# Optimization experiments

Hardware: AMD Instinct MI355X
Metric: run time of the kernel (lower is better)

The kernel has to match this reference:

```python
import jax, jax.numpy as jnp
import numpy as np

B, C, H, W = 16, 512, 14, 14
OUT = 8192
EPS_SQRT = 1e-5
EPS_NORM = 1e-12


def _make_sketch(key, input_dim, output_dim):
    kh, ks = jax.random.split(key)
    rand_h = jax.random.randint(kh, (input_dim,), 0, output_dim)
    rand_s = (2 * jax.random.randint(ks, (input_dim,), 0, 2) - 1).astype(jnp.float32)
    # count-sketch matrix densified: one nonzero (+-1) per row
    S = jnp.zeros((input_dim, output_dim), dtype=jnp.float32)
    return S.at[jnp.arange(input_dim), rand_h].set(rand_s)


def setup_inputs() -> dict:
    key = jax.random.key(0)
    kx, k1, k2 = jax.random.split(key, 3)
    x = jax.random.normal(kx, (B, C, H, W), dtype=jnp.float32)
    sketch1 = _make_sketch(k1, C, OUT)
    sketch2 = _make_sketch(k2, C, OUT)
    return {"x": x, "sketch1": sketch1, "sketch2": sketch2}


def reference(x, sketch1, sketch2):
    output_dim = sketch1.shape[1]
    # [B,C,H,W] -> [B,H,W,C] then project with count-sketch matrices -> [B,H,W,OUT]
    xp = jnp.transpose(x, (0, 2, 3, 1))
    p1 = xp @ sketch1
    p2 = xp @ sketch2
    # circular convolution via FFT (torch.rfft unnormalized; torch.irfft has 1/n, then *output_dim)
    f1 = jnp.fft.rfft(p1, axis=-1)
    f2 = jnp.fft.rfft(p2, axis=-1)
    cbp = jnp.fft.irfft(f1 * f2, n=output_dim, axis=-1) * output_dim
    # sum-pool over spatial dims -> [B, OUT]
    X = cbp.sum(axis=(1, 2))
    # signed square-root
    X = jnp.sign(X) * jnp.sqrt(jnp.abs(X) + EPS_SQRT)
    # L2 normalize per row (F.normalize semantics)
    norm = jnp.maximum(jnp.linalg.norm(X, axis=-1, keepdims=True), EPS_NORM)
    return X / norm
```

## Files before the change

kernel.cpp:

```cpp
#include <hip/hip_runtime.h>
#include <math.h>

#define OUT_DIM 8192
#define C_DIM   512
#define B_DIM   16
#define HW      196

typedef __attribute__((ext_vector_type(8))) short bf16x8;
typedef __attribute__((ext_vector_type(4))) float f32x4;


__global__ __launch_bounds__(256) void prep(
    const float* __restrict__ x,
    const float* __restrict__ S1, const float* __restrict__ S2,
    int* __restrict__ h1, float* __restrict__ s1,
    int* __restrict__ h2, float* __restrict__ s2,
    unsigned short* __restrict__ PH, unsigned short* __restrict__ PLo,
    float* __restrict__ ss)
{
    const int bid = blockIdx.x;
    const int t = threadIdx.x;

    if (bid < 1024) {
        int row = bid & 511;
        const float* S = (bid < 512) ? S1 : S2;
        int* h = (bid < 512) ? h1 : h2;
        float* s = (bid < 512) ? s1 : s2;
        const float4* p = (const float4*)(S + (size_t)row * OUT_DIM);
#pragma unroll
        for (int m = 0; m < 8; ++m) {
            int q = t + m * 256;
            float4 v = p[q];
            int base = q * 4;
            if (v.x != 0.f) { h[row] = base + 0; s[row] = v.x; }
            if (v.y != 0.f) { h[row] = base + 1; s[row] = v.y; }
            if (v.z != 0.f) { h[row] = base + 2; s[row] = v.z; }
            if (v.w != 0.f) { h[row] = base + 3; s[row] = v.w; }
        }
        if (bid == 0 && t < B_DIM) ss[t] = 0.f;
        return;
    }

    const int u = bid - 1024;
    const int b = u >> 5, rb = u & 31;
    __shared__ float xs[16 * HW];
    const float* src = x + ((size_t)b * C_DIM + rb * 16) * HW;
#pragma unroll
    for (int i = 0; i < 13; ++i) {
        int idx = t + i * 256;
        if (idx < 16 * HW) xs[idx] = src[idx];
    }
    __syncthreads();

    const int r = t & 15, u0 = t >> 4;
#pragma unroll
    for (int p = 0; p < 2; ++p) {
        int unit = u0 + p * 16;
        if (unit < 28) {
            bf16x8 hv, lv;
#pragma unroll
            for (int e = 0; e < 8; ++e) {
                int k = unit * 8 + e;
                float v = (k < HW) ? xs[r * HW + k] : 0.f;
                unsigned int uv = __float_as_uint(v);
                unsigned short hi = (unsigned short)(uv >> 16);
                float hif = __uint_as_float(((unsigned int)hi) << 16);
                hv[e] = (short)hi;
                lv[e] = (short)(__float_as_uint(v - hif) >> 16);
            }
            int kb = unit >> 2, lk = unit & 3;
            size_t base = ((((size_t)b * 32 + rb) * 7 + kb) * 4 + lk) * 128 + r * 8;
            *(bf16x8*)(PH + base) = hv;
            *(bf16x8*)(PLo + base) = lv;
        }
    }
}

__global__ __launch_bounds__(256) void gram_mfma(
    const unsigned short* __restrict__ PH, const unsigned short* __restrict__ PLo,
    const int* __restrict__ h1, const float* __restrict__ s1,
    const int* __restrict__ h2, const float* __restrict__ s2,
    float* __restrict__ partials)
{
    __shared__ float bins[OUT_DIM];

    const int bid = blockIdx.x;
    const int xcd = bid & 7;
    const int idx = bid >> 3;
    const int b   = xcd + 8 * (idx & 1);
    const int tile = idx >> 1;
    const int c1b = (tile >> 2) * 128, c2b = (tile & 3) * 128;

    const int t = threadIdx.x;
    const int l = t & 63, w = t >> 6;
    const int wr = w >> 1, wc = w & 1;

    for (int mm = t; mm < OUT_DIM; mm += 256) bins[mm] = 0.f;

    const size_t arb0 = ((size_t)b * 32 + (c1b >> 4) + wr * 4) * 7;
    const size_t brb0 = ((size_t)b * 32 + (c2b >> 4) + wc * 4) * 7;
    const int loff = l * 8;

#define FRAG(P, rbase, m, kb) (*(const bf16x8*)((P) + ((rbase) + (size_t)(m) * 7 + (kb)) * 512 + loff))

    f32x4 acc[4][4];
#pragma unroll
    for (int m = 0; m < 4; ++m)
#pragma unroll
        for (int n = 0; n < 4; ++n) acc[m][n] = (f32x4){0.f, 0.f, 0.f, 0.f};

    bf16x8 ah[2][4], al[2][4], bh[2][4], bl[2][4];
#pragma unroll
    for (int m = 0; m < 4; ++m) {
        ah[0][m] = FRAG(PH,  arb0, m, 0);
        al[0][m] = FRAG(PLo, arb0, m, 0);
        bh[0][m] = FRAG(PH,  brb0, m, 0);
        bl[0][m] = FRAG(PLo, brb0, m, 0);
    }

#pragma unroll
    for (int kb = 0; kb < 7; ++kb) {
        const int cur = kb & 1, nxt = cur ^ 1;
        if (kb < 6) {
#pragma unroll
            for (int m = 0; m < 4; ++m) {
                ah[nxt][m] = FRAG(PH,  arb0, m, kb + 1);
                al[nxt][m] = FRAG(PLo, arb0, m, kb + 1);
                bh[nxt][m] = FRAG(PH,  brb0, m, kb + 1);
                bl[nxt][m] = FRAG(PLo, brb0, m, kb + 1);
            }
        }
#pragma unroll
        for (int m = 0; m < 4; ++m)
#pragma unroll
            for (int n = 0; n < 4; ++n) {
                acc[m][n] = __builtin_amdgcn_mfma_f32_16x16x32_bf16(ah[cur][m], bh[cur][n], acc[m][n], 0, 0, 0);
                acc[m][n] = __builtin_amdgcn_mfma_f32_16x16x32_bf16(ah[cur][m], bl[cur][n], acc[m][n], 0, 0, 0);
                acc[m][n] = __builtin_amdgcn_mfma_f32_16x16x32_bf16(al[cur][m], bh[cur][n], acc[m][n], 0, 0, 0);
            }
    }
#undef FRAG

    const int lrow = l & 15, lk = l >> 4;
    int   hh1[4][4]; float sv1[4][4];
    int   hh2[4];    float sv2[4];
#pragma unroll
    for (int m = 0; m < 4; ++m)
#pragma unroll
        for (int r = 0; r < 4; ++r) {
            int c1 = c1b + wr * 64 + m * 16 + lk * 4 + r;
            hh1[m][r] = h1[c1]; sv1[m][r] = s1[c1];
        }
#pragma unroll
    for (int n = 0; n < 4; ++n) {
        int c2 = c2b + wc * 64 + n * 16 + lrow;
        hh2[n] = h2[c2]; sv2[n] = s2[c2];
    }

    __syncthreads();
#pragma unroll
    for (int m = 0; m < 4; ++m)
#pragma unroll
        for (int n = 0; n < 4; ++n)
#pragma unroll
            for (int r = 0; r < 4; ++r) {
                int bin = (hh1[m][r] + hh2[n]) & (OUT_DIM - 1);
                atomicAdd(&bins[bin], acc[m][n][r] * sv1[m][r] * sv2[n]);
            }
    __syncthreads();

    float* outp = partials + (size_t)(b * 16 + tile) * OUT_DIM;
    for (int mm = t; mm < OUT_DIM; mm += 256) outp[mm] = bins[mm];
}

__global__ __launch_bounds__(256) void fin_a(
    float* __restrict__ partials, float* __restrict__ ss)
{
    const int b = blockIdx.x >> 4, ch = blockIdx.x & 15, t = threadIdx.x;
    float sq = 0.f;
    float vals[2];
    int ks[2];
#pragma unroll
    for (int i = 0; i < 2; ++i) {
        int k = ch * 512 + i * 256 + t;
        ks[i] = k;
        float a = 0.f;
#pragma unroll
        for (int tile = 0; tile < 16; ++tile)
            a += partials[(size_t)(b * 16 + tile) * OUT_DIM + k];
        a *= (float)OUT_DIM;
        float sg = (a > 0.f) ? 1.f : ((a < 0.f) ? -1.f : 0.f);
        vals[i] = sg * sqrtf(fabsf(a) + 1e-5f);
        sq += fabsf(a) + 1e-5f;
    }
#pragma unroll
    for (int off = 32; off; off >>= 1) sq += __shfl_down(sq, off, 64);
    __shared__ float red[4];
    if ((t & 63) == 0) red[t >> 6] = sq;
    __syncthreads();
    if (t == 0) atomicAdd(&ss[b], red[0] + red[1] + red[2] + red[3]);
#pragma unroll
    for (int i = 0; i < 2; ++i)
        partials[(size_t)(b * 16) * OUT_DIM + ks[i]] = vals[i];
}

__global__ __launch_bounds__(256) void fin_b(
    const float* __restrict__ partials, const float* __restrict__ ss,
    float* __restrict__ out)
{
    const int b = blockIdx.x >> 4, ch = blockIdx.x & 15, t = threadIdx.x;
    float inv = 1.f / fmaxf(sqrtf(ss[b]), 1e-12f);
#pragma unroll
    for (int i = 0; i < 2; ++i) {
        int k = ch * 512 + i * 256 + t;
        out[(size_t)b * OUT_DIM + k] = partials[(size_t)(b * 16) * OUT_DIM + k] * inv;
    }
}

extern "C" void kernel_launch(void* const* d_in, const int* in_sizes, int n_in,
                              void* d_out, int out_size, void* d_ws, size_t ws_size,
                              hipStream_t stream) {
    const float* x   = (const float*)d_in[0];
    const float* sk1 = (const float*)d_in[1];
    const float* sk2 = (const float*)d_in[2];

    char* ws = (char*)d_ws;
    int*   h1 = (int*)(ws);
    float* s1 = (float*)(ws + 2048);
    int*   h2 = (int*)(ws + 4096);
    float* s2 = (float*)(ws + 6144);
    float* ss = (float*)(ws + 8192);
    float* partials = (float*)(ws + 8448);
    unsigned short* PH  = (unsigned short*)(ws + 8397056);
    unsigned short* PLo = (unsigned short*)(ws + 15737088);

    prep<<<1536, 256, 0, stream>>>(x, sk1, sk2, h1, s1, h2, s2, PH, PLo, ss);
    gram_mfma<<<256, 256, 0, stream>>>(PH, PLo, h1, s1, h2, s2, partials);
    fin_a<<<256, 256, 0, stream>>>(partials, ss);
    fin_b<<<256, 256, 0, stream>>>(partials, ss, (float*)d_out);
}
```

Measured before the change: 121.1 us.

## Fuse finalization into gram kernel via last-block counter and widen to 512 threads

Folds the two finalization kernels into the gram kernel. A per-batch atomic counter picks the last of the 16 tile blocks, which sums the partials, applies the signed square root and the L2 normalization, and writes the output, removing two kernel launches. The gram kernel now runs 8 waves per block with half the N-tile each, giving more parallelism per block and fewer registers per thread. The cost is that only 16 blocks do the serialized final reduction, and cross-block visibility depends on threadfence. The squared norm is now computed from the rounded root values rather than from abs plus epsilon.

```diff
diff --git a/kernel.cpp b/kernel.cpp
--- a/kernel.cpp
+++ b/kernel.cpp
@@ -16,7 +16,7 @@
     int* __restrict__ h1, float* __restrict__ s1,
     int* __restrict__ h2, float* __restrict__ s2,
     unsigned short* __restrict__ PH, unsigned short* __restrict__ PLo,
-    float* __restrict__ ss)
+    int* __restrict__ cnt)
 {
     const int bid = blockIdx.x;
     const int t = threadIdx.x;
@@ -37,7 +37,7 @@
             if (v.z != 0.f) { h[row] = base + 2; s[row] = v.z; }
             if (v.w != 0.f) { h[row] = base + 3; s[row] = v.w; }
         }
-        if (bid == 0 && t < B_DIM) ss[t] = 0.f;
+        if (bid == 0 && t < B_DIM) cnt[t] = 0;
         return;
     }
 
@@ -76,13 +76,16 @@
     }
 }
 
-__global__ __launch_bounds__(256) void gram_mfma(
+__global__ __launch_bounds__(512) void gram_fused(
     const unsigned short* __restrict__ PH, const unsigned short* __restrict__ PLo,
     const int* __restrict__ h1, const float* __restrict__ s1,
     const int* __restrict__ h2, const float* __restrict__ s2,
-    float* __restrict__ partials)
+    float* __restrict__ partials, int* __restrict__ cnt,
+    float* __restrict__ out)
 {
     __shared__ float bins[OUT_DIM];
+    __shared__ float red[8];
+    __shared__ int lastflag;
 
     const int bid = blockIdx.x;
     const int xcd = bid & 7;
@@ -93,29 +96,32 @@
 
     const int t = threadIdx.x;
     const int l = t & 63, w = t >> 6;
-    const int wr = w >> 1, wc = w & 1;
-
-    for (int mm = t; mm < OUT_DIM; mm += 256) bins[mm] = 0.f;
+    const int wr = w >> 2, wc = w & 3;
+
+    for (int mm = t; mm < OUT_DIM; mm += 512) bins[mm] = 0.f;
 
     const size_t arb0 = ((size_t)b * 32 + (c1b >> 4) + wr * 4) * 7;
-    const size_t brb0 = ((size_t)b * 32 + (c2b >> 4) + wc * 4) * 7;
+    const size_t brb0 = ((size_t)b * 32 + (c2b >> 4) + wc * 2) * 7;
     const int loff = l * 8;
 
 #define FRAG(P, rbase, m, kb) (*(const bf16x8*)((P) + ((rbase) + (size_t)(m) * 7 + (kb)) * 512 + loff))
 
-    f32x4 acc[4][4];
+    f32x4 acc[4][2];
 #pragma unroll
     for (int m = 0; m < 4; ++m)
 #pragma unroll
-        for (int n = 0; n < 4; ++n) acc[m][n] = (f32x4){0.f, 0.f, 0.f, 0.f};
-
-    bf16x8 ah[2][4], al[2][4], bh[2][4], bl[2][4];
+        for (int n = 0; n < 2; ++n) acc[m][n] = (f32x4){0.f, 0.f, 0.f, 0.f};
+
+    bf16x8 ah[2][4], al[2][4], bh[2][2], bl[2][2];
 #pragma unroll
     for (int m = 0; m < 4; ++m) {
         ah[0][m] = FRAG(PH,  arb0, m, 0);
         al[0][m] = FRAG(PLo, arb0, m, 0);
-        bh[0][m] = FRAG(PH,  brb0, m, 0);
-        bl[0][m] = FRAG(PLo, brb0, m, 0);
+    }
+#pragma unroll
+    for (int n = 0; n < 2; ++n) {
+        bh[0][n] = FRAG(PH,  brb0, n, 0);
+        bl[0][n] = FRAG(PLo, brb0, n, 0);
     }
 
 #pragma unroll
@@ -126,14 +132,17 @@
             for (int m = 0; m < 4; ++m) {
                 ah[nxt][m] = FRAG(PH,  arb0, m, kb + 1);
                 al[nxt][m] = FRAG(PLo, arb0, m, kb + 1);
-                bh[nxt][m] = FRAG(PH,  brb0, m, kb + 1);
-                bl[nxt][m] = FRAG(PLo, brb0, m, kb + 1);
+            }
+#pragma unroll
+            for (int n = 0; n < 2; ++n) {
+                bh[nxt][n] = FRAG(PH,  brb0, n, kb + 1);
+                bl[nxt][n] = FRAG(PLo, brb0, n, kb + 1);
             }
         }
 #pragma unroll
         for (int m = 0; m < 4; ++m)
 #pragma unroll
-            for (int n = 0; n < 4; ++n) {
+            for (int n = 0; n < 2; ++n) {
                 acc[m][n] = __builtin_amdgcn_mfma_f32_16x16x32_bf16(ah[cur][m], bh[cur][n], acc[m][n], 0, 0, 0);
                 acc[m][n] = __builtin_amdgcn_mfma_f32_16x16x32_bf16(ah[cur][m], bl[cur][n], acc[m][n], 0, 0, 0);
                 acc[m][n] = __builtin_amdgcn_mfma_f32_16x16x32_bf16(al[cur][m], bh[cur][n], acc[m][n], 0, 0, 0);
@@ -143,7 +152,7 @@
 
     const int lrow = l & 15, lk = l >> 4;
     int   hh1[4][4]; float sv1[4][4];
-    int   hh2[4];    float sv2[4];
+    int   hh2[2];    float sv2[2];
 #pragma unroll
     for (int m = 0; m < 4; ++m)
 #pragma unroll
@@ -152,8 +161,8 @@
             hh1[m][r] = h1[c1]; sv1[m][r] = s1[c1];
         }
 #pragma unroll
-    for (int n = 0; n < 4; ++n) {
-        int c2 = c2b + wc * 64 + n * 16 + lrow;
+    for (int n = 0; n < 2; ++n) {
+        int c2 = c2b + wc * 32 + n * 16 + lrow;
         hh2[n] = h2[c2]; sv2[n] = s2[c2];
     }
 
@@ -161,7 +170,7 @@
 #pragma unroll
     for (int m = 0; m < 4; ++m)
 #pragma unroll
-        for (int n = 0; n < 4; ++n)
+        for (int n = 0; n < 2; ++n)
 #pragma unroll
             for (int r = 0; r < 4; ++r) {
                 int bin = (hh1[m][r] + hh2[n]) & (OUT_DIM - 1);
@@ -170,50 +179,51 @@
     __syncthreads();
 
     float* outp = partials + (size_t)(b * 16 + tile) * OUT_DIM;
-    for (int mm = t; mm < OUT_DIM; mm += 256) outp[mm] = bins[mm];
-}
-
-__global__ __launch_bounds__(256) void fin_a(
-    float* __restrict__ partials, float* __restrict__ ss)
-{
-    const int b = blockIdx.x >> 4, ch = blockIdx.x & 15, t = threadIdx.x;
+    for (int mm = t; mm < OUT_DIM; mm += 512) outp[mm] = bins[mm];
+
+    __threadfence();
+    __syncthreads();
+    if (t == 0) lastflag = (atomicAdd(&cnt[b], 1) == 15);
+    __syncthreads();
+    if (!lastflag) return;
+    __threadfence();
+
+    const float4* p4 = (const float4*)(partials + (size_t)b * 16 * OUT_DIM);
+    float4 va[4];
     float sq = 0.f;
-    float vals[2];
-    int ks[2];
-#pragma unroll
-    for (int i = 0; i < 2; ++i) {
-        int k = ch * 512 + i * 256 + t;
-        ks[i] = k;
-        float a = 0.f;
-#pragma unroll
-        for (int tile = 0; tile < 16; ++tile)
-            a += partials[(size_t)(b * 16 + tile) * OUT_DIM + k];
-        a *= (float)OUT_DIM;
-        float sg = (a > 0.f) ? 1.f : ((a < 0.f) ? -1.f : 0.f);
-        vals[i] = sg * sqrtf(fabsf(a) + 1e-5f);
-        sq += fabsf(a) + 1e-5f;
+#pragma unroll
+    for (int i = 0; i < 4; ++i) {
+        int q = t + i * 512;
+        float4 s = make_float4(0.f, 0.f, 0.f, 0.f);
+#pragma unroll
+        for (int tl = 0; tl < 16; ++tl) {
+            float4 v = p4[tl * 2048 + q];
+            s.x += v.x; s.y += v.y; s.z += v.z; s.w += v.w;
+        }
+        float comp[4] = {s.x, s.y, s.z, s.w};
+#pragma unroll
+        for (int e = 0; e < 4; ++e) {
+            float a = comp[e] * (float)OUT_DIM;
+            float sg = (a > 0.f) ? 1.f : ((a < 0.f) ? -1.f : 0.f);
+            comp[e] = sg * sqrtf(fabsf(a) + 1e-5f);
+            sq += comp[e] * comp[e];
+        }
+        va[i] = make_float4(comp[0], comp[1], comp[2], comp[3]);
     }
 #pragma unroll
     for (int off = 32; off; off >>= 1) sq += __shfl_down(sq, off, 64);
-    __shared__ float red[4];
-    if ((t & 63) == 0) red[t >> 6] = sq;
-    __syncthreads();
-    if (t == 0) atomicAdd(&ss[b], red[0] + red[1] + red[2] + red[3]);
-#pragma unroll
-    for (int i = 0; i < 2; ++i)
-        partials[(size_t)(b * 16) * OUT_DIM + ks[i]] = vals[i];
-}
-
-__global__ __launch_bounds__(256) void fin_b(
-    const float* __restrict__ partials, const float* __restrict__ ss,
-    float* __restrict__ out)
-{
-    const int b = blockIdx.x >> 4, ch = blockIdx.x & 15, t = threadIdx.x;
-    float inv = 1.f / fmaxf(sqrtf(ss[b]), 1e-12f);
-#pragma unroll
-    for (int i = 0; i < 2; ++i) {
-        int k = ch * 512 + i * 256 + t;
-        out[(size_t)b * OUT_DIM + k] = partials[(size_t)(b * 16) * OUT_DIM + k] * inv;
+    if (l == 0) red[w] = sq;
+    __syncthreads();
+    float tot = 0.f;
+#pragma unroll
+    for (int i = 0; i < 8; ++i) tot += red[i];
+    float inv = 1.f / fmaxf(sqrtf(tot), 1e-12f);
+
+    float4* o4 = (float4*)(out + (size_t)b * OUT_DIM);
+#pragma unroll
+    for (int i = 0; i < 4; ++i) {
+        int q = t + i * 512;
+        o4[q] = make_float4(va[i].x * inv, va[i].y * inv, va[i].z * inv, va[i].w * inv);
     }
 }
 
@@ -229,13 +239,11 @@
     float* s1 = (float*)(ws + 2048);
     int*   h2 = (int*)(ws + 4096);
     float* s2 = (float*)(ws + 6144);
-    float* ss = (float*)(ws + 8192);
+    int*   cnt = (int*)(ws + 8192);
     float* partials = (float*)(ws + 8448);
     unsigned short* PH  = (unsigned short*)(ws + 8397056);
     unsigned short* PLo = (unsigned short*)(ws + 15737088);
 
-    prep<<<1536, 256, 0, stream>>>(x, sk1, sk2, h1, s1, h2, s2, PH, PLo, ss);
-    gram_mfma<<<256, 256, 0, stream>>>(PH, PLo, h1, s1, h2, s2, partials);
-    fin_a<<<256, 256, 0, stream>>>(partials, ss);
-    fin_b<<<256, 256, 0, stream>>>(partials, ss, (float*)d_out);
+    prep<<<1536, 256, 0, stream>>>(x, sk1, sk2, h1, s1, h2, s2, PH, PLo, cnt);
+    gram_fused<<<256, 512, 0, stream>>>(PH, PLo, h1, s1, h2, s2, partials, cnt, (float*)d_out);
 }
```

After: 158.1 us. 1.31x slower.

## Split gram K-loop across two wave halves and merge finalize kernels

Applied to the files above, without the earlier changes.

The gram kernel now runs 512 threads per block. Two groups of four waves each take half of the padded K range (8 blocks instead of 7, zero-padded), and both halves accumulate atomically into the same shared-memory bins. This doubles the waves available per CU to hide load latency. prep pads the bf16 layout to 8 k-blocks and drops the ss zeroing. The two finalize kernels are merged into one kernel with one 1024-thread block per batch, which removes a launch and the global atomic normalization pass. In exchange there are more shared-memory atomics, and the finalize runs on only 16 blocks.

```diff
diff --git a/kernel.cpp b/kernel.cpp
--- a/kernel.cpp
+++ b/kernel.cpp
@@ -15,8 +15,7 @@
     const float* __restrict__ S1, const float* __restrict__ S2,
     int* __restrict__ h1, float* __restrict__ s1,
     int* __restrict__ h2, float* __restrict__ s2,
-    unsigned short* __restrict__ PH, unsigned short* __restrict__ PLo,
-    float* __restrict__ ss)
+    unsigned short* __restrict__ PH, unsigned short* __restrict__ PLo)
 {
     const int bid = blockIdx.x;
     const int t = threadIdx.x;
@@ -37,7 +36,6 @@
             if (v.z != 0.f) { h[row] = base + 2; s[row] = v.z; }
             if (v.w != 0.f) { h[row] = base + 3; s[row] = v.w; }
         }
-        if (bid == 0 && t < B_DIM) ss[t] = 0.f;
         return;
     }
 
@@ -56,27 +54,25 @@
 #pragma unroll
     for (int p = 0; p < 2; ++p) {
         int unit = u0 + p * 16;
-        if (unit < 28) {
-            bf16x8 hv, lv;
-#pragma unroll
-            for (int e = 0; e < 8; ++e) {
-                int k = unit * 8 + e;
-                float v = (k < HW) ? xs[r * HW + k] : 0.f;
-                unsigned int uv = __float_as_uint(v);
-                unsigned short hi = (unsigned short)(uv >> 16);
-                float hif = __uint_as_float(((unsigned int)hi) << 16);
-                hv[e] = (short)hi;
-                lv[e] = (short)(__float_as_uint(v - hif) >> 16);
-            }
-            int kb = unit >> 2, lk = unit & 3;
-            size_t base = ((((size_t)b * 32 + rb) * 7 + kb) * 4 + lk) * 128 + r * 8;
-            *(bf16x8*)(PH + base) = hv;
-            *(bf16x8*)(PLo + base) = lv;
-        }
-    }
-}
-
-__global__ __launch_bounds__(256) void gram_mfma(
+        bf16x8 hv, lv;
+#pragma unroll
+        for (int e = 0; e < 8; ++e) {
+            int k = unit * 8 + e;
+            float v = (k < HW) ? xs[r * HW + k] : 0.f;
+            unsigned int uv = __float_as_uint(v);
+            unsigned short hi = (unsigned short)(uv >> 16);
+            float hif = __uint_as_float(((unsigned int)hi) << 16);
+            hv[e] = (short)hi;
+            lv[e] = (short)(__float_as_uint(v - hif) >> 16);
+        }
+        int kb = unit >> 2, lk = unit & 3;
+        size_t base = ((((size_t)b * 32 + rb) * 8 + kb) * 4 + lk) * 128 + r * 8;
+        *(bf16x8*)(PH + base) = hv;
+        *(bf16x8*)(PLo + base) = lv;
+    }
+}
+
+__global__ __launch_bounds__(512, 2) void gram_mfma(
     const unsigned short* __restrict__ PH, const unsigned short* __restrict__ PLo,
     const int* __restrict__ h1, const float* __restrict__ s1,
     const int* __restrict__ h2, const float* __restrict__ s2,
@@ -93,15 +89,17 @@
 
     const int t = threadIdx.x;
     const int l = t & 63, w = t >> 6;
-    const int wr = w >> 1, wc = w & 1;
-
-    for (int mm = t; mm < OUT_DIM; mm += 256) bins[mm] = 0.f;
-
-    const size_t arb0 = ((size_t)b * 32 + (c1b >> 4) + wr * 4) * 7;
-    const size_t brb0 = ((size_t)b * 32 + (c2b >> 4) + wc * 4) * 7;
+    const int half = w >> 2;
+    const int wr = (w >> 1) & 1, wc = w & 1;
+
+    for (int mm = t; mm < OUT_DIM; mm += 512) bins[mm] = 0.f;
+
+    const int arb = b * 32 + (c1b >> 4) + wr * 4;
+    const int brb = b * 32 + (c2b >> 4) + wc * 4;
     const int loff = l * 8;
-
-#define FRAG(P, rbase, m, kb) (*(const bf16x8*)((P) + ((rbase) + (size_t)(m) * 7 + (kb)) * 512 + loff))
+    const int kb0 = half * 4;
+
+#define FRAG(P, rb, kb) (*(const bf16x8*)((P) + ((size_t)((rb) * 8 + (kb)) * 512) + loff))
 
     f32x4 acc[4][4];
 #pragma unroll
@@ -112,22 +110,23 @@
     bf16x8 ah[2][4], al[2][4], bh[2][4], bl[2][4];
 #pragma unroll
     for (int m = 0; m < 4; ++m) {
-        ah[0][m] = FRAG(PH,  arb0, m, 0);
-        al[0][m] = FRAG(PLo, arb0, m, 0);
-        bh[0][m] = FRAG(PH,  brb0, m, 0);
-        bl[0][m] = FRAG(PLo, brb0, m, 0);
-    }
-
-#pragma unroll
-    for (int kb = 0; kb < 7; ++kb) {
-        const int cur = kb & 1, nxt = cur ^ 1;
-        if (kb < 6) {
+        ah[0][m] = FRAG(PH,  arb + m, kb0);
+        al[0][m] = FRAG(PLo, arb + m, kb0);
+        bh[0][m] = FRAG(PH,  brb + m, kb0);
+        bl[0][m] = FRAG(PLo, brb + m, kb0);
+    }
+
+#pragma unroll
+    for (int i = 0; i < 4; ++i) {
+        const int cur = i & 1, nxt = cur ^ 1;
+        if (i < 3) {
+            const int kn = kb0 + i + 1;
 #pragma unroll
             for (int m = 0; m < 4; ++m) {
-                ah[nxt][m] = FRAG(PH,  arb0, m, kb + 1);
-                al[nxt][m] = FRAG(PLo, arb0, m, kb + 1);
-                bh[nxt][m] = FRAG(PH,  brb0, m, kb + 1);
-                bl[nxt][m] = FRAG(PLo, brb0, m, kb + 1);
+                ah[nxt][m] = FRAG(PH,  arb + m, kn);
+                al[nxt][m] = FRAG(PLo, arb + m, kn);
+                bh[nxt][m] = FRAG(PH,  brb + m, kn);
+                bl[nxt][m] = FRAG(PLo, brb + m, kn);
             }
         }
 #pragma unroll
@@ -170,51 +169,40 @@
     __syncthreads();
 
     float* outp = partials + (size_t)(b * 16 + tile) * OUT_DIM;
-    for (int mm = t; mm < OUT_DIM; mm += 256) outp[mm] = bins[mm];
-}
-
-__global__ __launch_bounds__(256) void fin_a(
-    float* __restrict__ partials, float* __restrict__ ss)
+    for (int mm = t; mm < OUT_DIM; mm += 512) outp[mm] = bins[mm];
+}
+
+__global__ __launch_bounds__(1024) void fin(
+    const float* __restrict__ partials, float* __restrict__ out)
 {
-    const int b = blockIdx.x >> 4, ch = blockIdx.x & 15, t = threadIdx.x;
+    const int b = blockIdx.x, t = threadIdx.x;
+    const float* pb = partials + (size_t)b * 16 * OUT_DIM;
+    float v[8];
     float sq = 0.f;
-    float vals[2];
-    int ks[2];
-#pragma unroll
-    for (int i = 0; i < 2; ++i) {
-        int k = ch * 512 + i * 256 + t;
-        ks[i] = k;
+#pragma unroll
+    for (int i = 0; i < 8; ++i) {
+        int k = t + i * 1024;
         float a = 0.f;
 #pragma unroll
-        for (int tile = 0; tile < 16; ++tile)
-            a += partials[(size_t)(b * 16 + tile) * OUT_DIM + k];
+        for (int tl = 0; tl < 16; ++tl)
+            a += pb[tl * OUT_DIM + k];
         a *= (float)OUT_DIM;
         float sg = (a > 0.f) ? 1.f : ((a < 0.f) ? -1.f : 0.f);
-        vals[i] = sg * sqrtf(fabsf(a) + 1e-5f);
+        v[i] = sg * sqrtf(fabsf(a) + 1e-5f);
         sq += fabsf(a) + 1e-5f;
     }
 #pragma unroll
     for (int off = 32; off; off >>= 1) sq += __shfl_down(sq, off, 64);
-    __shared__ float red[4];
+    __shared__ float red[16];
     if ((t & 63) == 0) red[t >> 6] = sq;
     __syncthreads();
-    if (t == 0) atomicAdd(&ss[b], red[0] + red[1] + red[2] + red[3]);
-#pragma unroll
-    for (int i = 0; i < 2; ++i)
-        partials[(size_t)(b * 16) * OUT_DIM + ks[i]] = vals[i];
-}
-
-__global__ __launch_bounds__(256) void fin_b(
-    const float* __restrict__ partials, const float* __restrict__ ss,
-    float* __restrict__ out)
-{
-    const int b = blockIdx.x >> 4, ch = blockIdx.x & 15, t = threadIdx.x;
-    float inv = 1.f / fmaxf(sqrtf(ss[b]), 1e-12f);
-#pragma unroll
-    for (int i = 0; i < 2; ++i) {
-        int k = ch * 512 + i * 256 + t;
-        out[(size_t)b * OUT_DIM + k] = partials[(size_t)(b * 16) * OUT_DIM + k] * inv;
-    }
+    float tot = 0.f;
+#pragma unroll
+    for (int i = 0; i < 16; ++i) tot += red[i];
+    float inv = 1.f / fmaxf(sqrtf(tot), 1e-12f);
+#pragma unroll
+    for (int i = 0; i < 8; ++i)
+        out[(size_t)b * OUT_DIM + t + i * 1024] = v[i] * inv;
 }
 
 extern "C" void kernel_launch(void* const* d_in, const int* in_sizes, int n_in,
@@ -229,13 +217,11 @@
     float* s1 = (float*)(ws + 2048);
     int*   h2 = (int*)(ws + 4096);
     float* s2 = (float*)(ws + 6144);
-    float* ss = (float*)(ws + 8192);
-    float* partials = (float*)(ws + 8448);
-    unsigned short* PH  = (unsigned short*)(ws + 8397056);
-    unsigned short* PLo = (unsigned short*)(ws + 15737088);
-
-    prep<<<1536, 256, 0, stream>>>(x, sk1, sk2, h1, s1, h2, s2, PH, PLo, ss);
-    gram_mfma<<<256, 256, 0, stream>>>(PH, PLo, h1, s1, h2, s2, partials);
-    fin_a<<<256, 256, 0, stream>>>(partials, ss);
-    fin_b<<<256, 256, 0, stream>>>(partials, ss, (float*)d_out);
-}
+    float* partials = (float*)(ws + 8192);
+    unsigned short* PH  = (unsigned short*)(ws + 8396800);
+    unsigned short* PLo = (unsigned short*)(ws + 12591104);
+
+    prep<<<1536, 256, 0, stream>>>(x, sk1, sk2, h1, s1, h2, s2, PH, PLo);
+    gram_mfma<<<256, 512, 0, stream>>>(PH, PLo, h1, s1, h2, s2, partials);
+    fin<<<B_DIM, 1024, 0, stream>>>(partials, (float*)d_out);
+}
```

New measurement: 140.7 us. +16.2%, slower.
